# Kernel optimization log

Measured on AMD Instinct MI355X. Metric: run time of the kernel, lower is better.

Reference implementation:

```python
import jax, jax.numpy as jnp
import numpy as np

HIDDEN = 2304
HEADS = 16
THETA = 10000.0
LN_EPS = 1e-5


def setup_inputs() -> dict:
    key = jax.random.key(0)
    ks = jax.random.split(key, 6)
    d = HIDDEN
    init = lambda k, shape: jax.random.normal(k, shape, jnp.float32) * 0.02
    return {
        "x": jax.random.normal(ks[0], (4, 2048, d), jnp.float32),
        "wq": init(ks[1], (d, d)), "bq": jnp.zeros((d,), jnp.float32),
        "wk": init(ks[2], (d, d)), "bk": jnp.zeros((d,), jnp.float32),
        "wv": init(ks[3], (d, d)), "bv": jnp.zeros((d,), jnp.float32),
        "wo": init(ks[4], (d, d)), "bo": jnp.zeros((d,), jnp.float32),
        "ln_g": jnp.ones((d,), jnp.float32),
        "ln_b": jnp.zeros((d,), jnp.float32),
    }


def reference(x, wq, bq, wk, bk, wv, bv, wo, bo, ln_g, ln_b):
    b, s, d = x.shape
    H = HEADS
    Dh = d // H

    # qkv projections (nn.Linear: x @ W^T + b)
    q = jnp.einsum('bsd,ed->bse', x, wq) + bq
    k = jnp.einsum('bsd,ed->bse', x, wk) + bk
    v = jnp.einsum('bsd,ed->bse', x, wv) + bv

    # RoPE over the FULL hidden dim (d/2 pairs), as in the source
    pos = jnp.arange(s, dtype=jnp.float32)                    # (s,)
    scale = jnp.arange(0, d, 2, dtype=jnp.float32) / d        # (d/2,)
    omega = 1.0 / (THETA ** scale)                            # (d/2,)
    ang = pos[:, None] * omega[None, :]                       # (s, d/2)
    cos, sin = jnp.cos(ang), jnp.sin(ang)

    def rot(t):
        t2 = t.reshape(b, s, d // 2, 2)
        x0, x1 = t2[..., 0], t2[..., 1]
        return jnp.stack([cos * x0 - sin * x1, sin * x0 + cos * x1], axis=-1).reshape(b, s, d)

    q, k = rot(q), rot(k)

    # split heads -> (b, H, s, Dh)
    q = q.reshape(b, s, H, Dh).transpose(0, 2, 1, 3)
    k = k.reshape(b, s, H, Dh).transpose(0, 2, 1, 3)
    v = v.reshape(b, s, H, Dh).transpose(0, 2, 1, 3)

    # NOTE: faithful to source: einsum labels make this HEAD-mixing
    # attention at each position: logits shape (b, H, s, H)
    att_scale = 1.0 / (Dh ** 0.5)
    logits = jnp.einsum('bnhd,bmhd->bnhm', q, k) * att_scale
    w = jax.nn.softmax(logits, axis=-1)                       # (b,H,s,H)
    out = jnp.einsum('bnhm,bmhd->bnhd', w, v)                 # (b,H,s,Dh)

    out = out.transpose(0, 2, 1, 3).reshape(b, s, d)
    out = jnp.einsum('bsd,ed->bse', out, wo) + bo

    # residual + LayerNorm (dropout in eval mode -> identity)
    y = x + out
    mu = jnp.mean(y, axis=-1, keepdims=True)
    var = jnp.mean((y - mu) ** 2, axis=-1, keepdims=True)
    return (y - mu) * jax.lax.rsqrt(var + LN_EPS) * ln_g + ln_b
```

## Files before the change

kernel.cpp:

```cpp
#include <hip/hip_runtime.h>
#include <stdint.h>
#include <stddef.h>

#define D_HID 2304
#define NTOK  8192
#define NQKV  6912
#define WELEMS 5308416
#define SEQ_MASK 2047

typedef unsigned short u16;
typedef __bf16 bf16x8 __attribute__((ext_vector_type(8)));
typedef float  f32x16 __attribute__((ext_vector_type(16)));
typedef float  f32x4  __attribute__((ext_vector_type(4)));

__device__ __forceinline__ u16 f2bf(float f) {
    unsigned int u = __builtin_bit_cast(unsigned int, f);
    u += 0x7fffu + ((u >> 16) & 1u);
    return (u16)(u >> 16);
}
__device__ __forceinline__ float bf2f(u16 h) {
    unsigned int u = ((unsigned int)h) << 16;
    return __builtin_bit_cast(float, u);
}

__device__ __forceinline__ void gl2lds16(const void* g, void* l) {
    __builtin_amdgcn_global_load_lds(
        (const __attribute__((address_space(1))) void*)g,
        (__attribute__((address_space(3))) void*)l,
        16, 0, 0);
}

__global__ __launch_bounds__(256) void cvt_f32_bf16(
    const float* __restrict__ src, u16* __restrict__ dst)
{
    size_t i = ((size_t)blockIdx.x * 256 + threadIdx.x) * 4;
    float4 f = *(const float4*)(src + i);
    ushort4 o = make_ushort4(f2bf(f.x), f2bf(f.y), f2bf(f.z), f2bf(f.w));
    *(ushort4*)(dst + i) = o;
}

__global__ __launch_bounds__(256) void cvt_weights(
    const float* __restrict__ wq, const float* __restrict__ wk,
    const float* __restrict__ wv, const float* __restrict__ wo,
    u16* __restrict__ dst,
    const float* __restrict__ bq, const float* __restrict__ bk,
    const float* __restrict__ bv, float* __restrict__ bqkv)
{
    int i = blockIdx.x * 256 + threadIdx.x;
    if (i < NQKV)
        bqkv[i] = (i < 2304) ? bq[i] : (i < 4608) ? bk[i - 2304] : bv[i - 4608];
    size_t base = (size_t)i * 4;
    int r = (int)(base / WELEMS);
    const float* src = (r == 0) ? wq : (r == 1) ? wk : (r == 2) ? wv : wo;
    float4 f = *(const float4*)(src + (base - (size_t)r * WELEMS));
    ushort4 o = make_ushort4(f2bf(f.x), f2bf(f.y), f2bf(f.z), f2bf(f.w));
    *(ushort4*)(dst + base) = o;
}

__global__ __launch_bounds__(256) void rope_lut_k(float* __restrict__ lut)
{
    const float OMEGA_C = -2.0f * 13.287712379549449f / 2304.0f;
    const float INV2PI  = 0.15915494309189535f;
    const float fpos = (float)blockIdx.x;
    float* row = lut + (size_t)blockIdx.x * 2304;
    for (int p = threadIdx.x; p < 1152; p += 256) {
        float omega = exp2f((float)p * OMEGA_C);
        float rr = fpos * omega * INV2PI;
        rr -= floorf(rr);
        float sn = __builtin_amdgcn_sinf(rr);
        float cs = __builtin_amdgcn_cosf(rr);
        *(float2*)(row + 2 * p) = make_float2(cs, sn);
    }
}

__global__ __launch_bounds__(512, 2) void gemm256_bt(
    const u16* __restrict__ A, const u16* __restrict__ B,
    const float* __restrict__ bias, u16* __restrict__ Cout,
    int M, int N, int K)
{
    __shared__ __align__(16) u16 lds2[65536];

    const int tid  = threadIdx.x;
    const int lane = tid & 63;
    const int wave = tid >> 6;
    const int NT   = K >> 6;
    (void)M;

    const int chunk = gridDim.x >> 3;
    const int bid = (blockIdx.x & 7) * chunk + (blockIdx.x >> 3);
    const int num_bn = N >> 8;
    const int bm = bid / num_bn;
    const int bn = bid - bm * num_bn;

    const int srow = lane >> 3;
    const u16* __restrict__ Ast = A + (size_t)(bm * 256 + wave * 8 + srow) * K
                                    + ((lane & 7) ^ srow) * 8;
    const u16* __restrict__ Bst = B + (size_t)(bn * 256 + wave * 8 + srow) * K
                                    + ((lane & 7) ^ srow) * 8;
    const size_t row64  = (size_t)64 * K;
    const size_t row128 = (size_t)128 * K;
    const int ldsW = wave * 512;

#define STAGE(buf, hsel, tt) do {                                              \
    const u16* g_ = ((hsel) < 2 ? Ast : Bst)                                   \
                    + (((hsel) & 1) ? row128 : 0) + (size_t)(tt) * 64;         \
    u16* l_ = lds2 + (buf) * 32768 + (((hsel) < 2) ? 0 : 16384)                \
              + (((hsel) & 1) ? 8192 : 0) + ldsW;                              \
    gl2lds16(g_, l_);                                                          \
    gl2lds16(g_ + row64, l_ + 4096);                                           \
} while (0)

    const int l15 = lane & 15, l4 = lane >> 4;
    const int aBase = (wave >> 2) * 8192 + l15 * 64;
    const int bBase = 16384 + ((wave >> 1) & 1) * 8192
                      + ((wave & 1) * 64 + l15) * 64;
    const int s0 = ((l4    ) ^ (lane & 7)) * 8;
    const int s1 = ((l4 + 4) ^ (lane & 7)) * 8;

    f32x4 acc[8][4] = {};
    bf16x8 Bk0[4], Bk1[4], Aev[4], Aod[4];

    STAGE(0, 2, 0); STAGE(0, 3, 0); STAGE(0, 0, 0); STAGE(0, 1, 0);
    STAGE(1, 2, 1); STAGE(1, 3, 1); STAGE(1, 0, 1);
    asm volatile("s_waitcnt vmcnt(6)" ::: "memory");
    __builtin_amdgcn_s_barrier();
#pragma unroll
    for (int n = 0; n < 4; ++n)
        Bk0[n] = *(const bf16x8*)(lds2 + bBase + n * 1024 + s0);
#pragma unroll
    for (int mo = 0; mo < 4; ++mo)
        Aev[mo] = *(const bf16x8*)(lds2 + aBase + mo * 1024 + s0);

    for (int t = 0; t < NT; ++t) {
        const int cur = t & 1;
        const u16* lc = lds2 + cur * 32768;
        const u16* ln = lds2 + (cur ^ 1) * 32768;
        const bool st1 = (t + 1 < NT);
        const bool st2 = (t + 2 < NT);

#pragma unroll
        for (int n = 0; n < 4; ++n)
            Bk1[n] = *(const bf16x8*)(lc + bBase + n * 1024 + s1);
#pragma unroll
        for (int mo = 0; mo < 4; ++mo)
            Aod[mo] = *(const bf16x8*)(lc + aBase + (4 + mo) * 1024 + s0);
        if (st1) STAGE(cur ^ 1, 1, t + 1);
        __builtin_amdgcn_sched_barrier(0);
        __builtin_amdgcn_s_setprio(1);
#pragma unroll
        for (int mo = 0; mo < 4; ++mo)
#pragma unroll
            for (int n = 0; n < 4; ++n)
                acc[mo][n] = __builtin_amdgcn_mfma_f32_16x16x32_bf16(
                    Aev[mo], Bk0[n], acc[mo][n], 0, 0, 0);
        __builtin_amdgcn_s_setprio(0);
        __builtin_amdgcn_sched_barrier(0);
        __builtin_amdgcn_s_barrier();

#pragma unroll
        for (int mo = 0; mo < 4; ++mo)
            Aev[mo] = *(const bf16x8*)(lc + aBase + mo * 1024 + s1);
        if (st2) STAGE(cur, 2, t + 2);
        __builtin_amdgcn_sched_barrier(0);
        __builtin_amdgcn_s_setprio(1);
#pragma unroll
        for (int mo = 0; mo < 4; ++mo)
#pragma unroll
            for (int n = 0; n < 4; ++n)
                acc[4 + mo][n] = __builtin_amdgcn_mfma_f32_16x16x32_bf16(
                    Aod[mo], Bk0[n], acc[4 + mo][n], 0, 0, 0);
        __builtin_amdgcn_s_setprio(0);
        __builtin_amdgcn_sched_barrier(0);
        asm volatile("s_waitcnt lgkmcnt(0)" ::: "memory");
        __builtin_amdgcn_s_barrier();

#pragma unroll
        for (int mo = 0; mo < 4; ++mo)
            Aod[mo] = *(const bf16x8*)(lc + aBase + (4 + mo) * 1024 + s1);
        if (st2) STAGE(cur, 3, t + 2);
        if (st2)      asm volatile("s_waitcnt vmcnt(4)" ::: "memory");
        else if (st1) asm volatile("s_waitcnt vmcnt(0)" ::: "memory");
        __builtin_amdgcn_sched_barrier(0);
        __builtin_amdgcn_s_setprio(1);
#pragma unroll
        for (int mo = 0; mo < 4; ++mo)
#pragma unroll
            for (int n = 0; n < 4; ++n)
                acc[mo][n] = __builtin_amdgcn_mfma_f32_16x16x32_bf16(
                    Aev[mo], Bk1[n], acc[mo][n], 0, 0, 0);
        __builtin_amdgcn_s_setprio(0);
        __builtin_amdgcn_sched_barrier(0);
        asm volatile("s_waitcnt lgkmcnt(0)" ::: "memory");
        __builtin_amdgcn_s_barrier();

        if (st1) {
#pragma unroll
            for (int n = 0; n < 4; ++n)
                Bk0[n] = *(const bf16x8*)(ln + bBase + n * 1024 + s0);
#pragma unroll
            for (int mo = 0; mo < 4; ++mo)
                Aev[mo] = *(const bf16x8*)(ln + aBase + mo * 1024 + s0);
        }
        if (st2) STAGE(cur, 0, t + 2);
        __builtin_amdgcn_sched_barrier(0);
        __builtin_amdgcn_s_setprio(1);
#pragma unroll
        for (int mo = 0; mo < 4; ++mo)
#pragma unroll
            for (int n = 0; n < 4; ++n)
                acc[4 + mo][n] = __builtin_amdgcn_mfma_f32_16x16x32_bf16(
                    Aod[mo], Bk1[n], acc[4 + mo][n], 0, 0, 0);
        __builtin_amdgcn_s_setprio(0);
        __builtin_amdgcn_sched_barrier(0);
        asm volatile("s_waitcnt lgkmcnt(0)" ::: "memory");
        __builtin_amdgcn_s_barrier();
    }
#undef STAGE

    const int wm0 = (wave >> 2) * 128, wn0 = (wave & 3) * 64;
#pragma unroll
    for (int n = 0; n < 4; ++n) {
        const int gn = bn * 256 + wn0 + n * 16 + l15;
        const float bv = bias[gn];
#pragma unroll
        for (int m = 0; m < 8; ++m) {
            const int gm = bm * 256 + wm0 + m * 16 + l4 * 4;
#pragma unroll
            for (int j = 0; j < 4; ++j)
                Cout[(size_t)(gm + j) * N + gn] = f2bf(acc[m][n][j] + bv);
        }
    }
}

template<int MODE>
__global__ __launch_bounds__(256, 3) void gemm_bt(
    const u16* __restrict__ A, const u16* __restrict__ B,
    const float* __restrict__ bias, u16* __restrict__ Cout,
    const u16* __restrict__ resid, int M, int N, int K)
{
    __shared__ __align__(16) u16 As[128 * 64];
    __shared__ __align__(16) u16 Bs[128 * 64];

    const int tid  = threadIdx.x;
    const int lane = tid & 63;
    const int wave = tid >> 6;

    const int num_bn = N >> 7;
    const int rem = blockIdx.x % (num_bn << 3);
    const int bn  = rem >> 3;
    const int bm  = ((blockIdx.x / (num_bn << 3)) << 3) + (rem & 7);

    const int srow = tid >> 3;
    const int sc   = (tid & 7) ^ (srow & 7);
    const u16* Ag = A + (size_t)(bm * 128 + srow) * K + sc * 8;
    const u16* Bg = B + (size_t)(bn * 128 + srow) * K + sc * 8;
    const size_t row32 = (size_t)32 * K;
    u16* asd = As + wave * 512;
    u16* bsd = Bs + wave * 512;

    const int rl = lane & 31;
    const int h  = lane >> 5;
    const int swz = rl & 7;
    const int wm = (wave >> 1) * 64;
    const int wn = (wave & 1) * 64;

    f32x16 acc[2][2] = {};

    for (int kb = 0; kb < K; kb += 64) {
        __syncthreads();
#pragma unroll
        for (int r = 0; r < 4; ++r) {
            gl2lds16(Ag + kb + r * row32, asd + r * 2048);
            gl2lds16(Bg + kb + r * row32, bsd + r * 2048);
        }
        __syncthreads();

#pragma unroll
        for (int s = 0; s < 4; ++s) {
            const int ch = ((s * 2 + h) ^ swz) * 8;
            bf16x8 a0 = *(const bf16x8*)(As + (wm      + rl) * 64 + ch);
            bf16x8 a1 = *(const bf16x8*)(As + (wm + 32 + rl) * 64 + ch);
            bf16x8 b0 = *(const bf16x8*)(Bs + (wn      + rl) * 64 + ch);
            bf16x8 b1 = *(const bf16x8*)(Bs + (wn + 32 + rl) * 64 + ch);
            acc[0][0] = __builtin_amdgcn_mfma_f32_32x32x16_bf16(a0, b0, acc[0][0], 0, 0, 0);
            acc[0][1] = __builtin_amdgcn_mfma_f32_32x32x16_bf16(a0, b1, acc[0][1], 0, 0, 0);
            acc[1][0] = __builtin_amdgcn_mfma_f32_32x32x16_bf16(a1, b0, acc[1][0], 0, 0, 0);
            acc[1][1] = __builtin_amdgcn_mfma_f32_32x32x16_bf16(a1, b1, acc[1][1], 0, 0, 0);
        }
    }

#pragma unroll
    for (int mt = 0; mt < 2; ++mt) {
#pragma unroll
        for (int nt = 0; nt < 2; ++nt) {
            const int gn = bn * 128 + wn + nt * 32 + rl;
            const float bv = bias[gn];
#pragma unroll
            for (int reg = 0; reg < 16; ++reg) {
                const int gm = bm * 128 + wm + mt * 32 +
                               (reg & 3) + 8 * (reg >> 2) + 4 * h;
                const size_t idx = (size_t)gm * N + gn;
                float v = acc[mt][nt][reg] + bv;
                if constexpr (MODE == 1) v += bf2f(resid[idx]);
                Cout[idx] = f2bf(v);
            }
        }
    }
}

#define HROW 148
__global__ __launch_bounds__(256) void attn_headmix(
    const u16* __restrict__ QKV, const float* __restrict__ lut,
    u16* __restrict__ Aout)
{
    __shared__ __align__(16) float qs[16 * HROW];
    __shared__ __align__(16) float ks[16 * HROW];
    __shared__ __align__(16) float vs[16 * HROW];
    __shared__ __align__(16) float wsmT[256];

    const int tid = threadIdx.x;
    const int t   = blockIdx.x;
    const u16* row = QKV + (size_t)t * NQKV;
    const float* lutrow = lut + (size_t)(t & SEQ_MASK) * 2304;

    for (int c = tid; c < 864; c += 256) {
        uint4 raw = *(const uint4*)(row + c * 8);
        float f[8];
        f[0] = bf2f(raw.x & 0xffff); f[1] = bf2f(raw.x >> 16);
        f[2] = bf2f(raw.y & 0xffff); f[3] = bf2f(raw.y >> 16);
        f[4] = bf2f(raw.z & 0xffff); f[5] = bf2f(raw.z >> 16);
        f[6] = bf2f(raw.w & 0xffff); f[7] = bf2f(raw.w >> 16);
        if (c < 576) {
            const int cc = (c < 288) ? c : c - 288;
            const float4 t0 = *(const float4*)(lutrow + cc * 8);
            const float4 t1 = *(const float4*)(lutrow + cc * 8 + 4);
            float x0, x1;
            x0 = f[0]; x1 = f[1]; f[0] = t0.x * x0 - t0.y * x1; f[1] = t0.y * x0 + t0.x * x1;
            x0 = f[2]; x1 = f[3]; f[2] = t0.z * x0 - t0.w * x1; f[3] = t0.w * x0 + t0.z * x1;
            x0 = f[4]; x1 = f[5]; f[4] = t1.x * x0 - t1.y * x1; f[5] = t1.y * x0 + t1.x * x1;
            x0 = f[6]; x1 = f[7]; f[6] = t1.z * x0 - t1.w * x1; f[7] = t1.w * x0 + t1.z * x1;
            const int hr = cc / 18, col = (cc - hr * 18) * 8;
            float* dst = ((c < 288) ? qs : ks) + hr * HROW + col;
            *(float4*)(dst)     = make_float4(f[0], f[1], f[2], f[3]);
            *(float4*)(dst + 4) = make_float4(f[4], f[5], f[6], f[7]);
        } else {
            const int cv = c - 576;
            const int hr = cv / 18, col = (cv - hr * 18) * 8;
            float* dst = vs + hr * HROW + col;
            *(float4*)(dst)     = make_float4(f[0], f[1], f[2], f[3]);
            *(float4*)(dst + 4) = make_float4(f[4], f[5], f[6], f[7]);
        }
    }
    __syncthreads();

    const int n = tid >> 4, m = tid & 15;
    const float* qr = qs + n * HROW;
    const float* kr = ks + m * HROW;
    float s = 0.f;
#pragma unroll
    for (int d = 0; d < 144; d += 4) {
        float4 qv = *(const float4*)(qr + d);
        float4 kv = *(const float4*)(kr + d);
        s += qv.x * kv.x + qv.y * kv.y + qv.z * kv.z + qv.w * kv.w;
    }
    s *= (1.0f / 12.0f);

    float mx = s;
#pragma unroll
    for (int off = 8; off >= 1; off >>= 1) mx = fmaxf(mx, __shfl_xor(mx, off));
    float e = __expf(s - mx);
    float sum = e;
#pragma unroll
    for (int off = 8; off >= 1; off >>= 1) sum += __shfl_xor(sum, off);
    wsmT[m * 16 + n] = e / sum;
    __syncthreads();

    if (tid < 144) {
        const int col4 = tid % 36;
        const int nq   = tid / 36;
        const int oc   = col4 * 4;
        float4 a0 = {0,0,0,0}, a1 = {0,0,0,0}, a2 = {0,0,0,0}, a3 = {0,0,0,0};
#pragma unroll
        for (int mm = 0; mm < 16; ++mm) {
            float4 w4 = *(const float4*)(wsmT + mm * 16 + nq * 4);
            float4 v4 = *(const float4*)(vs + mm * HROW + oc);
            a0.x += w4.x * v4.x; a0.y += w4.x * v4.y; a0.z += w4.x * v4.z; a0.w += w4.x * v4.w;
            a1.x += w4.y * v4.x; a1.y += w4.y * v4.y; a1.z += w4.y * v4.z; a1.w += w4.y * v4.w;
            a2.x += w4.z * v4.x; a2.y += w4.z * v4.y; a2.z += w4.z * v4.z; a2.w += w4.z * v4.w;
            a3.x += w4.w * v4.x; a3.y += w4.w * v4.y; a3.z += w4.w * v4.z; a3.w += w4.w * v4.w;
        }
        u16* orow = Aout + (size_t)t * D_HID;
        float4 accs[4] = {a0, a1, a2, a3};
#pragma unroll
        for (int i = 0; i < 4; ++i) {
            const int nn = nq * 4 + i;
            ushort4 o = make_ushort4(f2bf(accs[i].x), f2bf(accs[i].y),
                                     f2bf(accs[i].z), f2bf(accs[i].w));
            *(ushort4*)(orow + nn * 144 + oc) = o;
        }
    }
}

__global__ __launch_bounds__(256) void ln_kernel(
    const u16* __restrict__ Y, const float* __restrict__ g,
    const float* __restrict__ b, float* __restrict__ out)
{
    const int tid  = threadIdx.x;
    const u16* y = Y + (size_t)blockIdx.x * D_HID;
    uint4 raw = *(const uint4*)(y + tid * 8);
    u16 extra = y[2048 + tid];
    float v[9];
    v[0] = bf2f(raw.x & 0xffff); v[1] = bf2f(raw.x >> 16);
    v[2] = bf2f(raw.y & 0xffff); v[3] = bf2f(raw.y >> 16);
    v[4] = bf2f(raw.z & 0xffff); v[5] = bf2f(raw.z >> 16);
    v[6] = bf2f(raw.w & 0xffff); v[7] = bf2f(raw.w >> 16);
    v[8] = bf2f(extra);
    float s = 0.f, s2 = 0.f;
#pragma unroll
    for (int r = 0; r < 9; ++r) { s += v[r]; s2 += v[r] * v[r]; }
#pragma unroll
    for (int off = 32; off >= 1; off >>= 1) {
        s  += __shfl_xor(s, off);
        s2 += __shfl_xor(s2, off);
    }
    __shared__ float red[8];
    const int wave = tid >> 6;
    if ((tid & 63) == 0) { red[wave] = s; red[4 + wave] = s2; }
    __syncthreads();
    s  = red[0] + red[1] + red[2] + red[3];
    s2 = red[4] + red[5] + red[6] + red[7];
    const float inv_n = 1.0f / 2304.0f;
    float mu  = s * inv_n;
    float var = fmaxf(s2 * inv_n - mu * mu, 0.f);
    float inv = rsqrtf(var + 1e-5f);
    float* orow = out + (size_t)blockIdx.x * D_HID;
    float4 g0 = *(const float4*)(g + tid * 8);
    float4 g1 = *(const float4*)(g + tid * 8 + 4);
    float4 b0 = *(const float4*)(b + tid * 8);
    float4 b1 = *(const float4*)(b + tid * 8 + 4);
    float4 o0, o1;
    o0.x = (v[0] - mu) * inv * g0.x + b0.x;
    o0.y = (v[1] - mu) * inv * g0.y + b0.y;
    o0.z = (v[2] - mu) * inv * g0.z + b0.z;
    o0.w = (v[3] - mu) * inv * g0.w + b0.w;
    o1.x = (v[4] - mu) * inv * g1.x + b1.x;
    o1.y = (v[5] - mu) * inv * g1.y + b1.y;
    o1.z = (v[6] - mu) * inv * g1.z + b1.z;
    o1.w = (v[7] - mu) * inv * g1.w + b1.w;
    *(float4*)(orow + tid * 8)     = o0;
    *(float4*)(orow + tid * 8 + 4) = o1;
    orow[2048 + tid] = (v[8] - mu) * inv * g[2048 + tid] + b[2048 + tid];
}

extern "C" void kernel_launch(void* const* d_in, const int* in_sizes, int n_in,
                              void* d_out, int out_size, void* d_ws, size_t ws_size,
                              hipStream_t stream)
{
    const float* x   = (const float*)d_in[0];
    const float* wq  = (const float*)d_in[1];
    const float* bq  = (const float*)d_in[2];
    const float* wk  = (const float*)d_in[3];
    const float* bk  = (const float*)d_in[4];
    const float* wv  = (const float*)d_in[5];
    const float* bv  = (const float*)d_in[6];
    const float* wo  = (const float*)d_in[7];
    const float* bo  = (const float*)d_in[8];
    const float* lng = (const float*)d_in[9];
    const float* lnb = (const float*)d_in[10];

    char* ws = (char*)d_ws;
    size_t off = 0;
    auto alloc = [&](size_t bytes) {
        void* p = ws + off;
        off += (bytes + 255) & ~(size_t)255;
        return p;
    };
    u16*   xb   = (u16*)alloc((size_t)NTOK * D_HID * 2);
    u16*   wqkv = (u16*)alloc((size_t)(NQKV + D_HID) * D_HID * 2);
    u16*   wob  = wqkv + (size_t)NQKV * D_HID;
    float* bqkv = (float*)alloc((size_t)NQKV * 4);
    u16*   qkv  = (u16*)alloc((size_t)NTOK * NQKV * 2);
    u16*   aout = (u16*)alloc((size_t)NTOK * D_HID * 2);
    float* lutw = (float*)alloc((size_t)2048 * 2304 * 4);
    u16*   ybuf = qkv;

    rope_lut_k<<<2048, 256, 0, stream>>>(lutw);
    cvt_f32_bf16<<<NTOK * D_HID / 1024, 256, 0, stream>>>(x, xb);
    cvt_weights<<<4 * WELEMS / 1024, 256, 0, stream>>>(wq, wk, wv, wo, wqkv,
                                                       bq, bk, bv, bqkv);
    gemm256_bt<<<(NTOK / 256) * (NQKV / 256), 512, 0, stream>>>(
        xb, wqkv, bqkv, qkv, NTOK, NQKV, D_HID);
    attn_headmix<<<NTOK, 256, 0, stream>>>(qkv, lutw, aout);
    gemm_bt<1><<<(D_HID / 128) * (NTOK / 128), 256, 0, stream>>>(
        aout, wob, bo, ybuf, xb, NTOK, D_HID, D_HID);
    ln_kernel<<<NTOK, 256, 0, stream>>>(ybuf, lng, lnb, (float*)d_out);
}
```

Before: 653.5 us.

## Rewrite head-mixing attention with bf16 MFMA, one token per wave

The per-token head-mixing attention kernel is replaced by one that gives each wavefront a single token. The 16x16 QK^T logits and the softmax-weighted V product are computed with 16x16x32 bf16 MFMA instructions instead of scalar fp32 dot products in LDS. RoPE is applied in registers, and V and the softmax weights are staged transposed in a small per-wave LDS region, so no block-wide barriers are needed. Q, K and softmax weights are now rounded to bf16 before the matrix ops, which lowers precision, and the output writes are scattered 2-byte stores.

Measured after the change: 653.4 us. About the same (-0.0%).

```diff
diff --git a/kernel.cpp b/kernel.cpp
--- a/kernel.cpp
+++ b/kernel.cpp
@@ -10,6 +10,7 @@
 
 typedef unsigned short u16;
 typedef __bf16 bf16x8 __attribute__((ext_vector_type(8)));
+typedef unsigned short ushort8 __attribute__((ext_vector_type(8)));
 typedef float  f32x16 __attribute__((ext_vector_type(16)));
 typedef float  f32x4  __attribute__((ext_vector_type(4)));
 
@@ -308,96 +309,97 @@
     }
 }
 
-#define HROW 148
-__global__ __launch_bounds__(256) void attn_headmix(
+__device__ __forceinline__ ushort8 rope8(ushort8 v, float4 t0, float4 t1) {
+    ushort8 o;
+    float x0, x1;
+    x0 = bf2f(v[0]); x1 = bf2f(v[1]);
+    o[0] = f2bf(t0.x * x0 - t0.y * x1); o[1] = f2bf(t0.y * x0 + t0.x * x1);
+    x0 = bf2f(v[2]); x1 = bf2f(v[3]);
+    o[2] = f2bf(t0.z * x0 - t0.w * x1); o[3] = f2bf(t0.w * x0 + t0.z * x1);
+    x0 = bf2f(v[4]); x1 = bf2f(v[5]);
+    o[4] = f2bf(t1.x * x0 - t1.y * x1); o[5] = f2bf(t1.y * x0 + t1.x * x1);
+    x0 = bf2f(v[6]); x1 = bf2f(v[7]);
+    o[6] = f2bf(t1.z * x0 - t1.w * x1); o[7] = f2bf(t1.w * x0 + t1.z * x1);
+    return o;
+}
+
+__global__ __launch_bounds__(512) void attn_mfma(
     const u16* __restrict__ QKV, const float* __restrict__ lut,
     u16* __restrict__ Aout)
 {
-    __shared__ __align__(16) float qs[16 * HROW];
-    __shared__ __align__(16) float ks[16 * HROW];
-    __shared__ __align__(16) float vs[16 * HROW];
-    __shared__ __align__(16) float wsmT[256];
-
-    const int tid = threadIdx.x;
-    const int t   = blockIdx.x;
+    __shared__ __align__(16) u16 smem[8 * 2688];
+    const int tid  = threadIdx.x;
+    const int lane = tid & 63;
+    const int wave = tid >> 6;
+    const int t    = blockIdx.x * 8 + wave;
+    const int l15  = lane & 15, l4 = lane >> 4;
+
+    u16* VT = smem + wave * 2688;
+    u16* WT = VT + 2304;
+
     const u16* row = QKV + (size_t)t * NQKV;
     const float* lutrow = lut + (size_t)(t & SEQ_MASK) * 2304;
 
-    for (int c = tid; c < 864; c += 256) {
-        uint4 raw = *(const uint4*)(row + c * 8);
-        float f[8];
-        f[0] = bf2f(raw.x & 0xffff); f[1] = bf2f(raw.x >> 16);
-        f[2] = bf2f(raw.y & 0xffff); f[3] = bf2f(raw.y >> 16);
-        f[4] = bf2f(raw.z & 0xffff); f[5] = bf2f(raw.z >> 16);
-        f[6] = bf2f(raw.w & 0xffff); f[7] = bf2f(raw.w >> 16);
-        if (c < 576) {
-            const int cc = (c < 288) ? c : c - 288;
-            const float4 t0 = *(const float4*)(lutrow + cc * 8);
-            const float4 t1 = *(const float4*)(lutrow + cc * 8 + 4);
-            float x0, x1;
-            x0 = f[0]; x1 = f[1]; f[0] = t0.x * x0 - t0.y * x1; f[1] = t0.y * x0 + t0.x * x1;
-            x0 = f[2]; x1 = f[3]; f[2] = t0.z * x0 - t0.w * x1; f[3] = t0.w * x0 + t0.z * x1;
-            x0 = f[4]; x1 = f[5]; f[4] = t1.x * x0 - t1.y * x1; f[5] = t1.y * x0 + t1.x * x1;
-            x0 = f[6]; x1 = f[7]; f[6] = t1.z * x0 - t1.w * x1; f[7] = t1.w * x0 + t1.z * x1;
-            const int hr = cc / 18, col = (cc - hr * 18) * 8;
-            float* dst = ((c < 288) ? qs : ks) + hr * HROW + col;
-            *(float4*)(dst)     = make_float4(f[0], f[1], f[2], f[3]);
-            *(float4*)(dst + 4) = make_float4(f[4], f[5], f[6], f[7]);
-        } else {
-            const int cv = c - 576;
-            const int hr = cv / 18, col = (cv - hr * 18) * 8;
-            float* dst = vs + hr * HROW + col;
-            *(float4*)(dst)     = make_float4(f[0], f[1], f[2], f[3]);
-            *(float4*)(dst + 4) = make_float4(f[4], f[5], f[6], f[7]);
-        }
-    }
-    __syncthreads();
-
-    const int n = tid >> 4, m = tid & 15;
-    const float* qr = qs + n * HROW;
-    const float* kr = ks + m * HROW;
-    float s = 0.f;
-#pragma unroll
-    for (int d = 0; d < 144; d += 4) {
-        float4 qv = *(const float4*)(qr + d);
-        float4 kv = *(const float4*)(kr + d);
-        s += qv.x * kv.x + qv.y * kv.y + qv.z * kv.z + qv.w * kv.w;
-    }
-    s *= (1.0f / 12.0f);
-
-    float mx = s;
-#pragma unroll
-    for (int off = 8; off >= 1; off >>= 1) mx = fmaxf(mx, __shfl_xor(mx, off));
-    float e = __expf(s - mx);
-    float sum = e;
-#pragma unroll
-    for (int off = 8; off >= 1; off >>= 1) sum += __shfl_xor(sum, off);
-    wsmT[m * 16 + n] = e / sum;
-    __syncthreads();
-
-    if (tid < 144) {
-        const int col4 = tid % 36;
-        const int nq   = tid / 36;
-        const int oc   = col4 * 4;
-        float4 a0 = {0,0,0,0}, a1 = {0,0,0,0}, a2 = {0,0,0,0}, a3 = {0,0,0,0};
-#pragma unroll
-        for (int mm = 0; mm < 16; ++mm) {
-            float4 w4 = *(const float4*)(wsmT + mm * 16 + nq * 4);
-            float4 v4 = *(const float4*)(vs + mm * HROW + oc);
-            a0.x += w4.x * v4.x; a0.y += w4.x * v4.y; a0.z += w4.x * v4.z; a0.w += w4.x * v4.w;
-            a1.x += w4.y * v4.x; a1.y += w4.y * v4.y; a1.z += w4.y * v4.z; a1.w += w4.y * v4.w;
-            a2.x += w4.z * v4.x; a2.y += w4.z * v4.y; a2.z += w4.z * v4.z; a2.w += w4.z * v4.w;
-            a3.x += w4.w * v4.x; a3.y += w4.w * v4.y; a3.z += w4.w * v4.z; a3.w += w4.w * v4.w;
-        }
-        u16* orow = Aout + (size_t)t * D_HID;
-        float4 accs[4] = {a0, a1, a2, a3};
-#pragma unroll
-        for (int i = 0; i < 4; ++i) {
-            const int nn = nq * 4 + i;
-            ushort4 o = make_ushort4(f2bf(accs[i].x), f2bf(accs[i].y),
-                                     f2bf(accs[i].z), f2bf(accs[i].w));
-            *(ushort4*)(orow + nn * 144 + oc) = o;
-        }
+    bf16x8 qf[5], kf[5];
+#pragma unroll
+    for (int kc = 0; kc < 5; ++kc) {
+        const int dbase = kc * 32 + l4 * 8;
+        ushort8 qv = {}, kv = {};
+        if (dbase < 144) {
+            qv = *(const ushort8*)(row + l15 * 144 + dbase);
+            kv = *(const ushort8*)(row + 2304 + l15 * 144 + dbase);
+            const float* lp = lutrow + l15 * 144 + dbase;
+            float4 c0 = *(const float4*)(lp);
+            float4 c1 = *(const float4*)(lp + 4);
+            qv = rope8(qv, c0, c1);
+            kv = rope8(kv, c0, c1);
+        }
+        qf[kc] = __builtin_bit_cast(bf16x8, qv);
+        kf[kc] = __builtin_bit_cast(bf16x8, kv);
+    }
+
+#pragma unroll
+    for (int kc = 0; kc < 5; ++kc) {
+        const int dbase = kc * 32 + l4 * 8;
+        if (dbase < 144) {
+            ushort8 vv = *(const ushort8*)(row + 4608 + l15 * 144 + dbase);
+#pragma unroll
+            for (int j = 0; j < 8; ++j)
+                VT[(dbase + j) * 16 + l15] = vv[j];
+        }
+    }
+
+    f32x4 S = {};
+#pragma unroll
+    for (int kc = 0; kc < 5; ++kc)
+        S = __builtin_amdgcn_mfma_f32_16x16x32_bf16(qf[kc], kf[kc], S, 0, 0, 0);
+
+#pragma unroll
+    for (int r = 0; r < 4; ++r) {
+        float s = S[r] * (1.0f / 12.0f);
+        float mx = s;
+#pragma unroll
+        for (int off = 8; off >= 1; off >>= 1) mx = fmaxf(mx, __shfl_xor(mx, off));
+        float e = __expf(s - mx);
+        float sum = e;
+#pragma unroll
+        for (int off = 8; off >= 1; off >>= 1) sum += __shfl_xor(sum, off);
+        WT[(l4 * 4 + r) * 24 + l15] = f2bf(e / sum);
+    }
+
+    bf16x8 wA = {};
+    if (l4 < 2) wA = *(const bf16x8*)(WT + l15 * 24 + l4 * 8);
+
+    u16* orow = Aout + (size_t)t * D_HID;
+#pragma unroll
+    for (int db = 0; db < 9; ++db) {
+        bf16x8 vB = {};
+        if (l4 < 2) vB = *(const bf16x8*)(VT + (db * 16 + l15) * 16 + l4 * 8);
+        f32x4 o = {};
+        o = __builtin_amdgcn_mfma_f32_16x16x32_bf16(wA, vB, o, 0, 0, 0);
+#pragma unroll
+        for (int r = 0; r < 4; ++r)
+            orow[(l4 * 4 + r) * 144 + db * 16 + l15] = f2bf(o[r]);
     }
 }
 
@@ -490,7 +492,7 @@
                                                        bq, bk, bv, bqkv);
     gemm256_bt<<<(NTOK / 256) * (NQKV / 256), 512, 0, stream>>>(
         xb, wqkv, bqkv, qkv, NTOK, NQKV, D_HID);
-    attn_headmix<<<NTOK, 256, 0, stream>>>(qkv, lutw, aout);
+    attn_mfma<<<NTOK / 8, 512, 0, stream>>>(qkv, lutw, aout);
     gemm_bt<1><<<(D_HID / 128) * (NTOK / 128), 256, 0, stream>>>(
         aout, wob, bo, ybuf, xb, NTOK, D_HID, D_HID);
     ln_kernel<<<NTOK, 256, 0, stream>>>(ybuf, lng, lnb, (float*)d_out);
```
